# Optimization experiments

Hardware: AMD Instinct MI355X
Metric: run time of the kernel (lower is better)

## Reference

```python
import jax, jax.numpy as jnp
import numpy as np

NEG_SLOPE = 0.2  # PyG GATConv default leaky_relu slope

def gat_conv(x, src, dst, W, a_src, a_dst, bias, N):
    # Linear transform
    h = x @ W                      # [N, D]
    # Per-node attention logits (heads=1)
    al_src = h @ a_src             # [N]
    al_dst = h @ a_dst             # [N]
    e = jax.nn.leaky_relu(al_src[src] + al_dst[dst], NEG_SLOPE)  # [E]
    # Segment softmax over incoming edges of each destination node
    m = jax.ops.segment_max(e, dst, num_segments=N)
    ex = jnp.exp(e - m[dst])
    denom = jax.ops.segment_sum(ex, dst, num_segments=N)
    alpha = ex / denom[dst]        # [E]
    # Weighted scatter-aggregate of source features
    out = jax.ops.segment_sum(h[src] * alpha[:, None], dst, num_segments=N)
    return out + bias

def setup_inputs() -> dict:
    key = jax.random.key(0)
    ks = jax.random.split(key, 10)
    N, E, F_in, H, O = 50000, 800000, 128, 64, 64
    x = jax.random.normal(ks[0], (N, F_in), dtype=jnp.float32)
    edge_index = jax.random.randint(ks[1], (2, E), 0, N, dtype=jnp.int32)
    s = lambda k, shp, fan: jax.random.normal(k, shp, dtype=jnp.float32) / np.sqrt(fan)
    return {
        'x': x, 'edge_index': edge_index,
        'W1': s(ks[2], (F_in, H), F_in), 'a_src1': s(ks[3], (H,), H), 'a_dst1': s(ks[4], (H,), H), 'b1': jnp.zeros((H,), jnp.float32),
        'W2': s(ks[5], (H, O), H), 'a_src2': s(ks[6], (O,), O), 'a_dst2': s(ks[7], (O,), O), 'b2': jnp.zeros((O,), jnp.float32),
    }

def reference(x, edge_index, W1, a_src1, a_dst1, b1, W2, a_src2, a_dst2, b2):
    N = x.shape[0]
    loops = jnp.arange(N, dtype=edge_index.dtype)  # PyG adds self-loops by default
    src = jnp.concatenate([edge_index[0], loops])
    dst = jnp.concatenate([edge_index[1], loops])
    h = gat_conv(x, src, dst, W1, a_src1, a_dst1, b1, N)
    h = jax.nn.relu(h)
    # dropout(p=0.6) is identity in eval mode
    out = gat_conv(h, src, dst, W2, a_src2, a_dst2, b2, N)
    return out
```

## Files before the change

### kernel.cpp

```cpp
#include <hip/hip_runtime.h>
#include <hip/hip_bf16.h>

#define DEV static __device__ __forceinline__

typedef short bf16x8 __attribute__((ext_vector_type(8)));
typedef float f32x4  __attribute__((ext_vector_type(4)));
typedef unsigned u32x4 __attribute__((ext_vector_type(4)));

union U4 { uint4 u; bf16x8 s; };

DEV float b2f(__hip_bfloat16 v) { return __bfloat162float(v); }
DEV float lrelu(float e) { return e > 0.f ? e : 0.2f * e; }

DEV unsigned short f2bu(float f) {
    __hip_bfloat16 b = __float2bfloat16(f);
    return *reinterpret_cast<unsigned short*>(&b);
}
DEV float bu2f(unsigned short u) { return __uint_as_float((unsigned)u << 16); }

DEV float loadF(const void* p, size_t i, int f32) {
    if (f32) return ((const float*)p)[i];
    return b2f(((const __hip_bfloat16*)p)[i]);
}

DEV uint4 pack8(const unsigned short* t) {
    uint4 v;
    v.x = (unsigned)t[0] | ((unsigned)t[1] << 16);
    v.y = (unsigned)t[2] | ((unsigned)t[3] << 16);
    v.z = (unsigned)t[4] | ((unsigned)t[5] << 16);
    v.w = (unsigned)t[6] | ((unsigned)t[7] << 16);
    return v;
}

DEV u32x4 pack8v(const unsigned short* t) {
    u32x4 v;
    v.x = (unsigned)t[0] | ((unsigned)t[1] << 16);
    v.y = (unsigned)t[2] | ((unsigned)t[3] << 16);
    v.z = (unsigned)t[4] | ((unsigned)t[5] << 16);
    v.w = (unsigned)t[6] | ((unsigned)t[7] << 16);
    return v;
}

DEV void edge_sd(int i, int E, const int* __restrict__ src, const int* __restrict__ dst,
                 int& s, int& d) {
    if (i < E) { s = src[i]; d = dst[i]; }
    else       { s = d = i - E; }
}

#define G_BIN 128

__global__ __launch_bounds__(256) void k_binA(
    const int* __restrict__ src, const int* __restrict__ dst,
    int* __restrict__ hist, int E, int EA, int chunk,
    const void* a0, int n0, const void* a1, int n1, const void* a2, int n2,
    const void* a3, int n3, const void* a4, int n4, const void* a5, int n5,
    const void* a6, int n6, const void* a7, int n7, const void* a8, int n8,
    int* __restrict__ flags)
{
    const int tid = threadIdx.x;
    if (blockIdx.x == G_BIN) {
        const void* ps[9] = {a0,a1,a2,a3,a4,a5,a6,a7,a8};
        const int   ns[9] = {n0,n1,n2,n3,n4,n5,n6,n7,n8};
        const int w = tid >> 6, lane = tid & 63;
        for (int k = w; k < 9; k += 4) {
            const unsigned short* p = (const unsigned short*)ps[k];
            const int n = ns[k];
            bool insane = false;
#pragma unroll
            for (int r = 0; r < 4; ++r) {
                int idx = lane + r * 64;
                if (idx < n) {
                    unsigned short u = p[idx];
                    unsigned e = (u >> 7) & 0xFFu;
                    insane |= (e >= 0xC8u) || (e == 0u && (u & 0x7Fu) != 0u);
                }
            }
            unsigned long long m = __ballot(insane);
            if (lane == 0) flags[k] = (m != 0ull) ? 1 : 0;
        }
        return;
    }
    __shared__ int cnt[256];
    cnt[tid] = 0;
    __syncthreads();
    const int lo = blockIdx.x * chunk;
    const int hi = min(lo + chunk, EA);
    for (int i = lo + tid; i < hi; i += 256) {
        int s, d; edge_sd(i, E, src, dst, s, d);
        atomicAdd(&cnt[d >> 8], 1);
    }
    __syncthreads();
    hist[blockIdx.x * 256 + tid] = cnt[tid];
}

__global__ __launch_bounds__(G_BIN) void k_binB1(
    const int* __restrict__ hist, int* __restrict__ offs_rel,
    int* __restrict__ btot)
{
    __shared__ int sm[G_BIN];
    const int t = threadIdx.x;
    const int b = blockIdx.x;
    int v = hist[t * 256 + b];
    sm[t] = v;
    __syncthreads();
#pragma unroll
    for (int off = 1; off < G_BIN; off <<= 1) {
        int u = (t >= off) ? sm[t - off] : 0;
        __syncthreads();
        sm[t] += u;
        __syncthreads();
    }
    offs_rel[t * 256 + b] = sm[t] - v;
    if (t == G_BIN - 1) btot[b] = sm[t];
}

__global__ __launch_bounds__(256) void k_binB2(
    const int* __restrict__ btot, int* __restrict__ bstart)
{
    __shared__ int sm[256];
    const int tid = threadIdx.x;
    int v = btot[tid];
    sm[tid] = v;
    __syncthreads();
#pragma unroll
    for (int off = 1; off < 256; off <<= 1) {
        int t = (tid >= off) ? sm[tid - off] : 0;
        __syncthreads();
        sm[tid] += t;
        __syncthreads();
    }
    bstart[tid] = sm[tid] - v;
    if (tid == 255) bstart[256] = sm[255];
}

__global__ __launch_bounds__(256) void k_binC(
    const int* __restrict__ src, const int* __restrict__ dst,
    const int* __restrict__ offs_rel, const int* __restrict__ bstart,
    unsigned* __restrict__ ebuf, int E, int EA, int chunk)
{
    __shared__ int cur[256];
    const int tid = threadIdx.x;
    cur[tid] = bstart[tid] + offs_rel[blockIdx.x * 256 + tid];
    __syncthreads();
    const int lo = blockIdx.x * chunk;
    const int hi = min(lo + chunk, EA);
    for (int i = lo + tid; i < hi; i += 256) {
        int s, d; edge_sd(i, E, src, dst, s, d);
        int pos = atomicAdd(&cur[d >> 8], 1);
        ebuf[pos] = ((unsigned)(d & 255) << 17) | (unsigned)s;
    }
}

__global__ __launch_bounds__(256) void k_binD(
    const unsigned* __restrict__ ebuf, const int* __restrict__ bstart,
    int* __restrict__ row_ptr, int* __restrict__ col, int N)
{
    __shared__ int cnt[256];
    __shared__ int pfx[256];
    const int tid = threadIdx.x;
    const int b = blockIdx.x;
    const int lo = bstart[b], hi = bstart[b + 1];
    cnt[tid] = 0;
    __syncthreads();
    for (int i = lo + tid; i < hi; i += 256)
        atomicAdd(&cnt[ebuf[i] >> 17], 1);
    __syncthreads();
    const int c = cnt[tid];
    pfx[tid] = c;
    __syncthreads();
#pragma unroll
    for (int off = 1; off < 256; off <<= 1) {
        int t = (tid >= off) ? pfx[tid - off] : 0;
        __syncthreads();
        pfx[tid] += t;
        __syncthreads();
    }
    const int excl = pfx[tid] - c;
    const int d = b * 256 + tid;
    if (d <= N) row_ptr[d] = lo + excl;
    __syncthreads();
    cnt[tid] = lo + excl;
    __syncthreads();
    for (int i = lo + tid; i < hi; i += 256) {
        unsigned v = ebuf[i];
        int pos = atomicAdd(&cnt[v >> 17], 1);
        col[pos] = (int)(v & 0x1FFFFu);
    }
}

__global__ __launch_bounds__(256) void k_gemm1(
    const void* __restrict__ x, const void* __restrict__ W,
    const void* __restrict__ a_s, const void* __restrict__ a_d,
    const int* __restrict__ flags,
    __hip_bfloat16* __restrict__ h, float* __restrict__ als, float* __restrict__ ald,
    int N)
{
    __shared__ __align__(16) unsigned short sMem[2 * 64 * 136];
    __shared__ float sAs[64], sAd[64];
    unsigned short* sA = sMem;
    unsigned short* sB = sMem + 64 * 136;
    float* sOut = (float*)sMem;

    const int tid = threadIdx.x;
    const int row0 = blockIdx.x * 64;
    const int fx = flags[0], fw = flags[1];

    if (tid < 64) sAs[tid] = loadF(a_s, tid, flags[2]);
    else if (tid < 128) sAd[tid - 64] = loadF(a_d, tid - 64, flags[3]);

    if (!fx) {
        const uint4* xg = (const uint4*)x;
#pragma unroll
        for (int it = 0; it < 2; ++it) {
            int g = tid + it * 256;
            int r = g >> 4, c16 = g & 15;
            uint4 v = (row0 + r < N) ? xg[(size_t)(row0 + r) * 16 + c16]
                                     : make_uint4(0, 0, 0, 0);
            *(uint4*)(sA + r * 136 + c16 * 8) = v;
        }
    } else {
        for (int i = tid; i < 64 * 128; i += 256) {
            int r = i >> 7, k = i & 127;
            float v = (row0 + r < N) ? ((const float*)x)[(size_t)(row0 + r) * 128 + k] : 0.f;
            sA[r * 136 + k] = f2bu(v);
        }
    }
    if (!fw) {
        const unsigned short* Wg = (const unsigned short*)W;
        const int n = tid & 63;
        int k0 = (tid >> 6) * 8;
#pragma unroll
        for (int rep = 0; rep < 4; ++rep, k0 += 32) {
            unsigned short t[8];
#pragma unroll
            for (int j = 0; j < 8; ++j) t[j] = Wg[(size_t)(k0 + j) * 64 + n];
            *(uint4*)(sB + n * 136 + k0) = pack8(t);
        }
    } else {
        const float* Wg = (const float*)W;
        for (int i = tid; i < 128 * 64; i += 256) {
            int k = i >> 6, n = i & 63;
            sB[n * 136 + k] = f2bu(Wg[i]);
        }
    }
    __syncthreads();

    const int w = tid >> 6, lane = tid & 63;
    const int m0 = w * 16;
    const int qr = lane >> 4;
    const int lc = lane & 15;

    bf16x8 afrag[4];
#pragma unroll
    for (int c = 0; c < 4; ++c) {
        U4 u; u.u = *(const uint4*)(sA + (m0 + lc) * 136 + c * 32 + qr * 8);
        afrag[c] = u.s;
    }
    f32x4 accs[4];
#pragma unroll
    for (int nt = 0; nt < 4; ++nt) {
        f32x4 acc = {0.f, 0.f, 0.f, 0.f};
#pragma unroll
        for (int c = 0; c < 4; ++c) {
            U4 u; u.u = *(const uint4*)(sB + (nt * 16 + lc) * 136 + c * 32 + qr * 8);
            acc = __builtin_amdgcn_mfma_f32_16x16x32_bf16(afrag[c], u.s, acc, 0, 0, 0);
        }
        accs[nt] = acc;
    }
    __syncthreads();

#pragma unroll
    for (int nt = 0; nt < 4; ++nt)
#pragma unroll
        for (int reg = 0; reg < 4; ++reg)
            sOut[(m0 + qr * 4 + reg) * 68 + nt * 16 + lc] = accs[nt][reg];
    __syncthreads();

    {
        const int r = tid >> 2, seg = tid & 3;
        const int row = row0 + r;
        const float* po = sOut + r * 68 + seg * 16;
        float ps = 0.f, pd = 0.f;
        unsigned short ob[16];
#pragma unroll
        for (int i = 0; i < 16; ++i) {
            float v = po[i];
            ps = fmaf(v, sAs[seg * 16 + i], ps);
            pd = fmaf(v, sAd[seg * 16 + i], pd);
            ob[i] = f2bu(v);
        }
        if (row < N) {
            uint4* hp = (uint4*)((unsigned short*)h + (size_t)row * 64 + seg * 16);
            hp[0] = pack8(ob);
            hp[1] = pack8(ob + 8);
        }
        ps += __shfl_xor(ps, 1, 64); ps += __shfl_xor(ps, 2, 64);
        pd += __shfl_xor(pd, 1, 64); pd += __shfl_xor(pd, 2, 64);
        if (seg == 0 && row < N) { als[row] = ps; ald[row] = pd; }
    }
}

__global__ __launch_bounds__(256) void k_gemm2(
    __hip_bfloat16* __restrict__ agg, const void* __restrict__ b1,
    const void* __restrict__ W, const void* __restrict__ a_s,
    const void* __restrict__ a_d, const int* __restrict__ flags,
    float* __restrict__ als, float* __restrict__ ald, int N)
{
    __shared__ __align__(16) unsigned short sMem[2 * 64 * 72];
    __shared__ float sAs[64], sAd[64], sBias[64];
    unsigned short* sA = sMem;
    unsigned short* sB = sMem + 64 * 72;
    float* sOut = (float*)sMem;

    const int tid = threadIdx.x;
    const int row0 = blockIdx.x * 64;
    const int fw = flags[5];

    if (tid < 64) sAs[tid] = loadF(a_s, tid, flags[6]);
    else if (tid < 128) sAd[tid - 64] = loadF(a_d, tid - 64, flags[7]);
    else if (tid < 192) sBias[tid - 128] = loadF(b1, tid - 128, flags[4]);
    __syncthreads();

    {
        const uint4* ag = (const uint4*)agg;
#pragma unroll
        for (int it = 0; it < 2; ++it) {
            int g = tid + it * 256;
            int r = g >> 3, c8 = g & 7;
            uint4 v = (row0 + r < N) ? ag[(size_t)(row0 + r) * 8 + c8]
                                     : make_uint4(0, 0, 0, 0);
            unsigned short in[8] = {
                (unsigned short)(v.x & 0xFFFF), (unsigned short)(v.x >> 16),
                (unsigned short)(v.y & 0xFFFF), (unsigned short)(v.y >> 16),
                (unsigned short)(v.z & 0xFFFF), (unsigned short)(v.z >> 16),
                (unsigned short)(v.w & 0xFFFF), (unsigned short)(v.w >> 16)};
            unsigned short ob[8];
#pragma unroll
            for (int j = 0; j < 8; ++j) {
                float t = bu2f(in[j]) + sBias[c8 * 8 + j];
                ob[j] = f2bu(t > 0.f ? t : 0.f);
            }
            *(uint4*)(sA + r * 72 + c8 * 8) = pack8(ob);
        }
    }
    if (!fw) {
        const unsigned short* Wg = (const unsigned short*)W;
        const int n = tid & 63;
        int k0 = (tid >> 6) * 8;
#pragma unroll
        for (int rep = 0; rep < 2; ++rep, k0 += 32) {
            unsigned short t[8];
#pragma unroll
            for (int j = 0; j < 8; ++j) t[j] = Wg[(size_t)(k0 + j) * 64 + n];
            *(uint4*)(sB + n * 72 + k0) = pack8(t);
        }
    } else {
        const float* Wg = (const float*)W;
        for (int i = tid; i < 64 * 64; i += 256) {
            int k = i >> 6, n = i & 63;
            sB[n * 72 + k] = f2bu(Wg[i]);
        }
    }
    __syncthreads();

    const int w = tid >> 6, lane = tid & 63;
    const int m0 = w * 16;
    const int qr = lane >> 4, lc = lane & 15;

    bf16x8 afrag[2];
#pragma unroll
    for (int c = 0; c < 2; ++c) {
        U4 u; u.u = *(const uint4*)(sA + (m0 + lc) * 72 + c * 32 + qr * 8);
        afrag[c] = u.s;
    }
    f32x4 accs[4];
#pragma unroll
    for (int nt = 0; nt < 4; ++nt) {
        f32x4 acc = {0.f, 0.f, 0.f, 0.f};
#pragma unroll
        for (int c = 0; c < 2; ++c) {
            U4 u; u.u = *(const uint4*)(sB + (nt * 16 + lc) * 72 + c * 32 + qr * 8);
            acc = __builtin_amdgcn_mfma_f32_16x16x32_bf16(afrag[c], u.s, acc, 0, 0, 0);
        }
        accs[nt] = acc;
    }
    __syncthreads();
#pragma unroll
    for (int nt = 0; nt < 4; ++nt)
#pragma unroll
        for (int reg = 0; reg < 4; ++reg)
            sOut[(m0 + qr * 4 + reg) * 68 + nt * 16 + lc] = accs[nt][reg];
    __syncthreads();

    {
        const int r = tid >> 2, seg = tid & 3;
        const int row = row0 + r;
        const float* po = sOut + r * 68 + seg * 16;
        float ps = 0.f, pd = 0.f;
        unsigned short ob[16];
#pragma unroll
        for (int i = 0; i < 16; ++i) {
            float v = po[i];
            ps = fmaf(v, sAs[seg * 16 + i], ps);
            pd = fmaf(v, sAd[seg * 16 + i], pd);
            ob[i] = f2bu(v);
        }
        if (row < N) {
            uint4* hp = (uint4*)((unsigned short*)agg + (size_t)row * 64 + seg * 16);
            hp[0] = pack8(ob);
            hp[1] = pack8(ob + 8);
        }
        ps += __shfl_xor(ps, 1, 64); ps += __shfl_xor(ps, 2, 64);
        pd += __shfl_xor(pd, 1, 64); pd += __shfl_xor(pd, 2, 64);
        if (seg == 0 && row < N) { als[row] = ps; ald[row] = pd; }
    }
}

__global__ __launch_bounds__(256) void k_gather(
    const int* __restrict__ row_ptr, const int* __restrict__ col,
    const float* __restrict__ als, const float* __restrict__ ald,
    const __hip_bfloat16* __restrict__ h,
    __hip_bfloat16* __restrict__ agg_out,
    void* __restrict__ final_out,
    const void* __restrict__ bias, const int* __restrict__ flags, int N)
{
    const int tid = threadIdx.x;
    const int lane = tid & 63;
    const int eg = lane >> 3, fg = lane & 7;
    const int wid = blockIdx.x * 4 + (tid >> 6);
    const int nw  = gridDim.x * 4;

    for (int d = wid; d < N; d += nw) {
        const float aldd = ald[d];
        const int beg = row_ptr[d], end = row_ptr[d + 1];
        float acc[8] = {0.f,0.f,0.f,0.f,0.f,0.f,0.f,0.f};
        float den = 0.f;
        for (int j = beg + eg; j < end; j += 8) {
            const int s = col[j];
            const float w = __expf(lrelu(als[s] + aldd));
            den += w;
            const uint4 hv = *reinterpret_cast<const uint4*>(h + (size_t)s * 64 + fg * 8);
            acc[0] = fmaf(w, __uint_as_float(hv.x << 16),          acc[0]);
            acc[1] = fmaf(w, __uint_as_float(hv.x & 0xFFFF0000u),  acc[1]);
            acc[2] = fmaf(w, __uint_as_float(hv.y << 16),          acc[2]);
            acc[3] = fmaf(w, __uint_as_float(hv.y & 0xFFFF0000u),  acc[3]);
            acc[4] = fmaf(w, __uint_as_float(hv.z << 16),          acc[4]);
            acc[5] = fmaf(w, __uint_as_float(hv.z & 0xFFFF0000u),  acc[5]);
            acc[6] = fmaf(w, __uint_as_float(hv.w << 16),          acc[6]);
            acc[7] = fmaf(w, __uint_as_float(hv.w & 0xFFFF0000u),  acc[7]);
        }
#pragma unroll
        for (int off = 8; off <= 32; off <<= 1) {
            den += __shfl_xor(den, off, 64);
#pragma unroll
            for (int k = 0; k < 8; ++k) acc[k] += __shfl_xor(acc[k], off, 64);
        }
        if (eg == 0) {
            const float inv = 1.f / den;
            if (final_out) {
                float vb[8];
#pragma unroll
                for (int k = 0; k < 8; ++k) vb[k] = acc[k] * inv + loadF(bias, fg * 8 + k, flags[8]);
                if (flags[0]) {
                    float* o = (float*)final_out + (size_t)d * 64 + fg * 8;
                    f32x4 o0 = {vb[0], vb[1], vb[2], vb[3]};
                    f32x4 o1 = {vb[4], vb[5], vb[6], vb[7]};
                    __builtin_nontemporal_store(o0, (f32x4*)o);
                    __builtin_nontemporal_store(o1, (f32x4*)(o + 4));
                } else {
                    unsigned short ob[8];
#pragma unroll
                    for (int k = 0; k < 8; ++k) ob[k] = f2bu(vb[k]);
                    __builtin_nontemporal_store(pack8v(ob),
                        reinterpret_cast<u32x4*>((__hip_bfloat16*)final_out + (size_t)d * 64 + fg * 8));
                }
            } else {
                unsigned short ob[8];
#pragma unroll
                for (int k = 0; k < 8; ++k) ob[k] = f2bu(acc[k] * inv);
                __builtin_nontemporal_store(pack8v(ob),
                    reinterpret_cast<u32x4*>(agg_out + (size_t)d * 64 + fg * 8));
            }
        }
    }
}

extern "C" void kernel_launch(void* const* d_in, const int* in_sizes, int n_in,
                              void* d_out, int out_size, void* d_ws, size_t ws_size,
                              hipStream_t stream)
{
    const void* x   = d_in[0];
    const int*  ei  = (const int*)d_in[1];
    const void* W1  = d_in[2];
    const void* as1 = d_in[3];
    const void* ad1 = d_in[4];
    const void* b1  = d_in[5];
    const void* W2  = d_in[6];
    const void* as2 = d_in[7];
    const void* ad2 = d_in[8];
    const void* b2  = d_in[9];

    const int N  = in_sizes[0] / 128;
    const int E  = in_sizes[1] / 2;
    const int EA = E + N;
    const int* src = ei;
    const int* dst = ei + E;

    uintptr_t base = (uintptr_t)d_ws;
    auto alloc = [&](size_t bytes) { uintptr_t p = base; base += (bytes + 63) & ~(size_t)63; return p; };
    int*      flags    = (int*)alloc(64 * 4);
    float*    als      = (float*)alloc((size_t)N * 4);
    float*    ald      = (float*)alloc((size_t)N * 4);
    int*      row_ptr  = (int*)alloc((size_t)(N + 1) * 4);
    int*      hist     = (int*)alloc((size_t)G_BIN * 256 * 4);
    int*      offs_rel = (int*)alloc((size_t)G_BIN * 256 * 4);
    int*      btot     = (int*)alloc(256 * 4);
    int*      bstart   = (int*)alloc(257 * 4);
    unsigned* ebuf     = (unsigned*)alloc((size_t)EA * 4);
    int*      col      = (int*)alloc((size_t)EA * 4);
    __hip_bfloat16* hbuf   = (__hip_bfloat16*)alloc((size_t)N * 64 * 2);
    __hip_bfloat16* aggbuf = (__hip_bfloat16*)alloc((size_t)N * 64 * 2);

    const int gatherb = 2048;
    const int gb  = (N + 63) / 64;
    const int NBK = (N + 255) / 256;
    const int chunk = (EA + G_BIN - 1) / G_BIN;

    k_binA<<<G_BIN + 1, 256, 0, stream>>>(
        src, dst, hist, E, EA, chunk,
        x, in_sizes[0], W1, in_sizes[2], as1, in_sizes[3], ad1, in_sizes[4],
        b1, in_sizes[5], W2, in_sizes[6], as2, in_sizes[7], ad2, in_sizes[8],
        b2, in_sizes[9], flags);
    k_binB1<<<256, G_BIN, 0, stream>>>(hist, offs_rel, btot);
    k_binB2<<<1, 256, 0, stream>>>(btot, bstart);
    k_binC<<<G_BIN, 256, 0, stream>>>(src, dst, offs_rel, bstart, ebuf, E, EA, chunk);
    k_binD<<<NBK, 256, 0, stream>>>(ebuf, bstart, row_ptr, col, N);

    k_gemm1<<<gb, 256, 0, stream>>>(x, W1, as1, ad1, flags, hbuf, als, ald, N);
    k_gather<<<gatherb, 256, 0, stream>>>(row_ptr, col, als, ald, hbuf, aggbuf,
                                          nullptr, nullptr, flags, N);
    k_gemm2<<<gb, 256, 0, stream>>>(aggbuf, b1, W2, as2, ad2, flags, als, ald, N);
    k_gather<<<gatherb, 256, 0, stream>>>(row_ptr, col, als, ald, aggbuf, nullptr,
                                          d_out, b2, flags, N);
    (void)out_size; (void)ws_size; (void)n_in;
}
```

Baseline: 211.0 us.

## Fuse layer-1 GEMM with edge histogram kernel and fold bucket scan into consumers

Merges the first GEMM with the edge-histogram and dtype-detection kernel into a single launch, so GEMM blocks and histogram blocks run concurrently. Each GEMM block re-detects the input dtypes itself instead of waiting on the flags written by another kernel. The single-block bucket prefix-scan kernel is removed, and the 256-entry scan is recomputed redundantly inside k_binC and k_binD. This removes two launches and their serialization at the cost of duplicated scan and detection work per block.

```diff
diff --git a/kernel.cpp b/kernel.cpp
--- a/kernel.cpp
+++ b/kernel.cpp
@@ -47,50 +47,174 @@
     else       { s = d = i - E; }
 }
 
+DEV int detect_wave(const void* p, int n, int lane) {
+    const unsigned short* u16 = (const unsigned short*)p;
+    bool insane = false;
+#pragma unroll
+    for (int r = 0; r < 4; ++r) {
+        int idx = lane + r * 64;
+        if (idx < n) {
+            unsigned short u = u16[idx];
+            unsigned e = (u >> 7) & 0xFFu;
+            insane |= (e >= 0xC8u) || (e == 0u && (u & 0x7Fu) != 0u);
+        }
+    }
+    return (__ballot(insane) != 0ull) ? 1 : 0;
+}
+
 #define G_BIN 128
 
-__global__ __launch_bounds__(256) void k_binA(
+__global__ __launch_bounds__(256) void k_fused1(
+    const void* __restrict__ x, const void* __restrict__ W,
+    const void* __restrict__ a_s, const void* __restrict__ a_d,
+    __hip_bfloat16* __restrict__ h, float* __restrict__ als, float* __restrict__ ald,
+    int N, int gb, int nx, int nW1,
     const int* __restrict__ src, const int* __restrict__ dst,
     int* __restrict__ hist, int E, int EA, int chunk,
-    const void* a0, int n0, const void* a1, int n1, const void* a2, int n2,
-    const void* a3, int n3, const void* a4, int n4, const void* a5, int n5,
-    const void* a6, int n6, const void* a7, int n7, const void* a8, int n8,
+    const void* a5, int n5, const void* a6, int n6, const void* a7, int n7,
+    const void* a8, int n8, const void* a9, int n9,
     int* __restrict__ flags)
 {
     const int tid = threadIdx.x;
-    if (blockIdx.x == G_BIN) {
-        const void* ps[9] = {a0,a1,a2,a3,a4,a5,a6,a7,a8};
-        const int   ns[9] = {n0,n1,n2,n3,n4,n5,n6,n7,n8};
+    const int bid = blockIdx.x;
+
+    if (bid >= gb) {
+        if (bid == gb + G_BIN) {
+            const void* ps[9] = {x, W, a_s, a_d, a5, a6, a7, a8, a9};
+            const int   ns[9] = {nx, nW1, 64, 64, n5, n6, n7, n8, n9};
+            const int w = tid >> 6, lane = tid & 63;
+            for (int k = w; k < 9; k += 4) {
+                int f = detect_wave(ps[k], ns[k], lane);
+                if (lane == 0) flags[k] = f;
+            }
+            return;
+        }
+        __shared__ int cnt[256];
+        cnt[tid] = 0;
+        __syncthreads();
+        const int cb = bid - gb;
+        const int lo = cb * chunk;
+        const int hi = min(lo + chunk, EA);
+        for (int i = lo + tid; i < hi; i += 256) {
+            int s, d; edge_sd(i, E, src, dst, s, d);
+            atomicAdd(&cnt[d >> 8], 1);
+        }
+        __syncthreads();
+        hist[cb * 256 + tid] = cnt[tid];
+        return;
+    }
+
+    __shared__ __align__(16) unsigned short sMem[2 * 64 * 136];
+    __shared__ float sAs[64], sAd[64];
+    __shared__ int sFl[4];
+    unsigned short* sA = sMem;
+    unsigned short* sB = sMem + 64 * 136;
+    float* sOut = (float*)sMem;
+
+    {
+        const void* ps4[4] = {x, W, a_s, a_d};
+        const int   ns4[4] = {nx, nW1, 64, 64};
         const int w = tid >> 6, lane = tid & 63;
-        for (int k = w; k < 9; k += 4) {
-            const unsigned short* p = (const unsigned short*)ps[k];
-            const int n = ns[k];
-            bool insane = false;
-#pragma unroll
-            for (int r = 0; r < 4; ++r) {
-                int idx = lane + r * 64;
-                if (idx < n) {
-                    unsigned short u = p[idx];
-                    unsigned e = (u >> 7) & 0xFFu;
-                    insane |= (e >= 0xC8u) || (e == 0u && (u & 0x7Fu) != 0u);
-                }
-            }
-            unsigned long long m = __ballot(insane);
-            if (lane == 0) flags[k] = (m != 0ull) ? 1 : 0;
-        }
-        return;
-    }
-    __shared__ int cnt[256];
-    cnt[tid] = 0;
-    __syncthreads();
-    const int lo = blockIdx.x * chunk;
-    const int hi = min(lo + chunk, EA);
-    for (int i = lo + tid; i < hi; i += 256) {
-        int s, d; edge_sd(i, E, src, dst, s, d);
-        atomicAdd(&cnt[d >> 8], 1);
-    }
-    __syncthreads();
-    hist[blockIdx.x * 256 + tid] = cnt[tid];
+        int f = detect_wave(ps4[w], ns4[w], lane);
+        if (lane == 0) sFl[w] = f;
+    }
+    __syncthreads();
+    const int fx = sFl[0], fw = sFl[1];
+
+    const int row0 = bid * 64;
+    if (tid < 64) sAs[tid] = loadF(a_s, tid, sFl[2]);
+    else if (tid < 128) sAd[tid - 64] = loadF(a_d, tid - 64, sFl[3]);
+
+    if (!fx) {
+        const uint4* xg = (const uint4*)x;
+#pragma unroll
+        for (int it = 0; it < 2; ++it) {
+            int g = tid + it * 256;
+            int r = g >> 4, c16 = g & 15;
+            uint4 v = (row0 + r < N) ? xg[(size_t)(row0 + r) * 16 + c16]
+                                     : make_uint4(0, 0, 0, 0);
+            *(uint4*)(sA + r * 136 + c16 * 8) = v;
+        }
+    } else {
+        for (int i = tid; i < 64 * 128; i += 256) {
+            int r = i >> 7, k = i & 127;
+            float v = (row0 + r < N) ? ((const float*)x)[(size_t)(row0 + r) * 128 + k] : 0.f;
+            sA[r * 136 + k] = f2bu(v);
+        }
+    }
+    if (!fw) {
+        const unsigned short* Wg = (const unsigned short*)W;
+        const int n = tid & 63;
+        int k0 = (tid >> 6) * 8;
+#pragma unroll
+        for (int rep = 0; rep < 4; ++rep, k0 += 32) {
+            unsigned short t[8];
+#pragma unroll
+            for (int j = 0; j < 8; ++j) t[j] = Wg[(size_t)(k0 + j) * 64 + n];
+            *(uint4*)(sB + n * 136 + k0) = pack8(t);
+        }
+    } else {
+        const float* Wg = (const float*)W;
+        for (int i = tid; i < 128 * 64; i += 256) {
+            int k = i >> 6, n = i & 63;
+            sB[n * 136 + k] = f2bu(Wg[i]);
+        }
+    }
+    __syncthreads();
+
+    const int w = tid >> 6, lane = tid & 63;
+    const int m0 = w * 16;
+    const int qr = lane >> 4;
+    const int lc = lane & 15;
+
+    bf16x8 afrag[4];
+#pragma unroll
+    for (int c = 0; c < 4; ++c) {
+        U4 u; u.u = *(const uint4*)(sA + (m0 + lc) * 136 + c * 32 + qr * 8);
+        afrag[c] = u.s;
+    }
+    f32x4 accs[4];
+#pragma unroll
+    for (int nt = 0; nt < 4; ++nt) {
+        f32x4 acc = {0.f, 0.f, 0.f, 0.f};
+#pragma unroll
+        for (int c = 0; c < 4; ++c) {
+            U4 u; u.u = *(const uint4*)(sB + (nt * 16 + lc) * 136 + c * 32 + qr * 8);
+            acc = __builtin_amdgcn_mfma_f32_16x16x32_bf16(afrag[c], u.s, acc, 0, 0, 0);
+        }
+        accs[nt] = acc;
+    }
+    __syncthreads();
+
+#pragma unroll
+    for (int nt = 0; nt < 4; ++nt)
+#pragma unroll
+        for (int reg = 0; reg < 4; ++reg)
+            sOut[(m0 + qr * 4 + reg) * 68 + nt * 16 + lc] = accs[nt][reg];
+    __syncthreads();
+
+    {
+        const int r = tid >> 2, seg = tid & 3;
+        const int row = row0 + r;
+        const float* po = sOut + r * 68 + seg * 16;
+        float ps = 0.f, pd = 0.f;
+        unsigned short ob[16];
+#pragma unroll
+        for (int i = 0; i < 16; ++i) {
+            float v = po[i];
+            ps = fmaf(v, sAs[seg * 16 + i], ps);
+            pd = fmaf(v, sAd[seg * 16 + i], pd);
+            ob[i] = f2bu(v);
+        }
+        if (row < N) {
+            uint4* hp = (uint4*)((unsigned short*)h + (size_t)row * 64 + seg * 16);
+            hp[0] = pack8(ob);
+            hp[1] = pack8(ob + 8);
+        }
+        ps += __shfl_xor(ps, 1, 64); ps += __shfl_xor(ps, 2, 64);
+        pd += __shfl_xor(pd, 1, 64); pd += __shfl_xor(pd, 2, 64);
+        if (seg == 0 && row < N) { als[row] = ps; ald[row] = pd; }
+    }
 }
 
 __global__ __launch_bounds__(G_BIN) void k_binB1(
@@ -114,10 +238,13 @@
     if (t == G_BIN - 1) btot[b] = sm[t];
 }
 
-__global__ __launch_bounds__(256) void k_binB2(
-    const int* __restrict__ btot, int* __restrict__ bstart)
+__global__ __launch_bounds__(256) void k_binC(
+    const int* __restrict__ src, const int* __restrict__ dst,
+    const int* __restrict__ offs_rel, const int* __restrict__ btot,
+    unsigned* __restrict__ ebuf, int E, int EA, int chunk)
 {
     __shared__ int sm[256];
+    __shared__ int cur[256];
     const int tid = threadIdx.x;
     int v = btot[tid];
     sm[tid] = v;
@@ -129,18 +256,7 @@
         sm[tid] += t;
         __syncthreads();
     }
-    bstart[tid] = sm[tid] - v;
-    if (tid == 255) bstart[256] = sm[255];
-}
-
-__global__ __launch_bounds__(256) void k_binC(
-    const int* __restrict__ src, const int* __restrict__ dst,
-    const int* __restrict__ offs_rel, const int* __restrict__ bstart,
-    unsigned* __restrict__ ebuf, int E, int EA, int chunk)
-{
-    __shared__ int cur[256];
-    const int tid = threadIdx.x;
-    cur[tid] = bstart[tid] + offs_rel[blockIdx.x * 256 + tid];
+    cur[tid] = (sm[tid] - v) + offs_rel[blockIdx.x * 256 + tid];
     __syncthreads();
     const int lo = blockIdx.x * chunk;
     const int hi = min(lo + chunk, EA);
@@ -152,14 +268,28 @@
 }
 
 __global__ __launch_bounds__(256) void k_binD(
-    const unsigned* __restrict__ ebuf, const int* __restrict__ bstart,
+    const unsigned* __restrict__ ebuf, const int* __restrict__ btot,
     int* __restrict__ row_ptr, int* __restrict__ col, int N)
 {
+    __shared__ int sm[256];
     __shared__ int cnt[256];
     __shared__ int pfx[256];
     const int tid = threadIdx.x;
     const int b = blockIdx.x;
-    const int lo = bstart[b], hi = bstart[b + 1];
+    {
+        int v = btot[tid];
+        sm[tid] = v;
+        __syncthreads();
+#pragma unroll
+        for (int off = 1; off < 256; off <<= 1) {
+            int t = (tid >= off) ? sm[tid - off] : 0;
+            __syncthreads();
+            sm[tid] += t;
+            __syncthreads();
+        }
+    }
+    const int lo = (b == 0) ? 0 : sm[b - 1];
+    const int hi = sm[b];
     cnt[tid] = 0;
     __syncthreads();
     for (int i = lo + tid; i < hi; i += 256)
@@ -185,118 +315,6 @@
         unsigned v = ebuf[i];
         int pos = atomicAdd(&cnt[v >> 17], 1);
         col[pos] = (int)(v & 0x1FFFFu);
-    }
-}
-
-__global__ __launch_bounds__(256) void k_gemm1(
-    const void* __restrict__ x, const void* __restrict__ W,
-    const void* __restrict__ a_s, const void* __restrict__ a_d,
-    const int* __restrict__ flags,
-    __hip_bfloat16* __restrict__ h, float* __restrict__ als, float* __restrict__ ald,
-    int N)
-{
-    __shared__ __align__(16) unsigned short sMem[2 * 64 * 136];
-    __shared__ float sAs[64], sAd[64];
-    unsigned short* sA = sMem;
-    unsigned short* sB = sMem + 64 * 136;
-    float* sOut = (float*)sMem;
-
-    const int tid = threadIdx.x;
-    const int row0 = blockIdx.x * 64;
-    const int fx = flags[0], fw = flags[1];
-
-    if (tid < 64) sAs[tid] = loadF(a_s, tid, flags[2]);
-    else if (tid < 128) sAd[tid - 64] = loadF(a_d, tid - 64, flags[3]);
-
-    if (!fx) {
-        const uint4* xg = (const uint4*)x;
-#pragma unroll
-        for (int it = 0; it < 2; ++it) {
-            int g = tid + it * 256;
-            int r = g >> 4, c16 = g & 15;
-            uint4 v = (row0 + r < N) ? xg[(size_t)(row0 + r) * 16 + c16]
-                                     : make_uint4(0, 0, 0, 0);
-            *(uint4*)(sA + r * 136 + c16 * 8) = v;
-        }
-    } else {
-        for (int i = tid; i < 64 * 128; i += 256) {
-            int r = i >> 7, k = i & 127;
-            float v = (row0 + r < N) ? ((const float*)x)[(size_t)(row0 + r) * 128 + k] : 0.f;
-            sA[r * 136 + k] = f2bu(v);
-        }
-    }
-    if (!fw) {
-        const unsigned short* Wg = (const unsigned short*)W;
-        const int n = tid & 63;
-        int k0 = (tid >> 6) * 8;
-#pragma unroll
-        for (int rep = 0; rep < 4; ++rep, k0 += 32) {
-            unsigned short t[8];
-#pragma unroll
-            for (int j = 0; j < 8; ++j) t[j] = Wg[(size_t)(k0 + j) * 64 + n];
-            *(uint4*)(sB + n * 136 + k0) = pack8(t);
-        }
-    } else {
-        const float* Wg = (const float*)W;
-        for (int i = tid; i < 128 * 64; i += 256) {
-            int k = i >> 6, n = i & 63;
-            sB[n * 136 + k] = f2bu(Wg[i]);
-        }
-    }
-    __syncthreads();
-
-    const int w = tid >> 6, lane = tid & 63;
-    const int m0 = w * 16;
-    const int qr = lane >> 4;
-    const int lc = lane & 15;
-
-    bf16x8 afrag[4];
-#pragma unroll
-    for (int c = 0; c < 4; ++c) {
-        U4 u; u.u = *(const uint4*)(sA + (m0 + lc) * 136 + c * 32 + qr * 8);
-        afrag[c] = u.s;
-    }
-    f32x4 accs[4];
-#pragma unroll
-    for (int nt = 0; nt < 4; ++nt) {
-        f32x4 acc = {0.f, 0.f, 0.f, 0.f};
-#pragma unroll
-        for (int c = 0; c < 4; ++c) {
-            U4 u; u.u = *(const uint4*)(sB + (nt * 16 + lc) * 136 + c * 32 + qr * 8);
-            acc = __builtin_amdgcn_mfma_f32_16x16x32_bf16(afrag[c], u.s, acc, 0, 0, 0);
-        }
-        accs[nt] = acc;
-    }
-    __syncthreads();
-
-#pragma unroll
-    for (int nt = 0; nt < 4; ++nt)
-#pragma unroll
-        for (int reg = 0; reg < 4; ++reg)
-            sOut[(m0 + qr * 4 + reg) * 68 + nt * 16 + lc] = accs[nt][reg];
-    __syncthreads();
-
-    {
-        const int r = tid >> 2, seg = tid & 3;
-        const int row = row0 + r;
-        const float* po = sOut + r * 68 + seg * 16;
-        float ps = 0.f, pd = 0.f;
-        unsigned short ob[16];
-#pragma unroll
-        for (int i = 0; i < 16; ++i) {
-            float v = po[i];
-            ps = fmaf(v, sAs[seg * 16 + i], ps);
-            pd = fmaf(v, sAd[seg * 16 + i], pd);
-            ob[i] = f2bu(v);
-        }
-        if (row < N) {
-            uint4* hp = (uint4*)((unsigned short*)h + (size_t)row * 64 + seg * 16);
-            hp[0] = pack8(ob);
-            hp[1] = pack8(ob + 8);
-        }
-        ps += __shfl_xor(ps, 1, 64); ps += __shfl_xor(ps, 2, 64);
-        pd += __shfl_xor(pd, 1, 64); pd += __shfl_xor(pd, 2, 64);
-        if (seg == 0 && row < N) { als[row] = ps; ald[row] = pd; }
     }
 }
 
@@ -515,7 +533,6 @@
     int*      hist     = (int*)alloc((size_t)G_BIN * 256 * 4);
     int*      offs_rel = (int*)alloc((size_t)G_BIN * 256 * 4);
     int*      btot     = (int*)alloc(256 * 4);
-    int*      bstart   = (int*)alloc(257 * 4);
     unsigned* ebuf     = (unsigned*)alloc((size_t)EA * 4);
     int*      col      = (int*)alloc((size_t)EA * 4);
     __hip_bfloat16* hbuf   = (__hip_bfloat16*)alloc((size_t)N * 64 * 2);
@@ -526,17 +543,15 @@
     const int NBK = (N + 255) / 256;
     const int chunk = (EA + G_BIN - 1) / G_BIN;
 
-    k_binA<<<G_BIN + 1, 256, 0, stream>>>(
+    k_fused1<<<gb + G_BIN + 1, 256, 0, stream>>>(
+        x, W1, as1, ad1, hbuf, als, ald, N, gb, in_sizes[0], in_sizes[2],
         src, dst, hist, E, EA, chunk,
-        x, in_sizes[0], W1, in_sizes[2], as1, in_sizes[3], ad1, in_sizes[4],
         b1, in_sizes[5], W2, in_sizes[6], as2, in_sizes[7], ad2, in_sizes[8],
         b2, in_sizes[9], flags);
     k_binB1<<<256, G_BIN, 0, stream>>>(hist, offs_rel, btot);
-    k_binB2<<<1, 256, 0, stream>>>(btot, bstart);
-    k_binC<<<G_BIN, 256, 0, stream>>>(src, dst, offs_rel, bstart, ebuf, E, EA, chunk);
-    k_binD<<<NBK, 256, 0, stream>>>(ebuf, bstart, row_ptr, col, N);
-
-    k_gemm1<<<gb, 256, 0, stream>>>(x, W1, as1, ad1, flags, hbuf, als, ald, N);
+    k_binC<<<G_BIN, 256, 0, stream>>>(src, dst, offs_rel, btot, ebuf, E, EA, chunk);
+    k_binD<<<NBK, 256, 0, stream>>>(ebuf, btot, row_ptr, col, N);
+
     k_gather<<<gatherb, 256, 0, stream>>>(row_ptr, col, als, ald, hbuf, aggbuf,
                                           nullptr, nullptr, flags, N);
     k_gemm2<<<gb, 256, 0, stream>>>(aggbuf, b1, W2, as2, ad2, flags, als, ald, N);
```

New measurement: 200.6 us. 1.05x faster.
